# Kernel tuning notes

Measured on AMD Instinct MI355X. Metric: run time of the kernel, lower is better.

The kernel has to match this reference:

```python
import jax, jax.numpy as jnp
import numpy as np

TOKENS = 8192
IN_F = 4096
OUT_F = 4096
QMAX = 127.0  # int8 symmetric quant range
EPS = 1e-8


def setup_inputs() -> dict:
    key = jax.random.key(0)
    k1, k2, k3, k4 = jax.random.split(key, 4)
    x = jax.random.normal(k1, (TOKENS, IN_F), dtype=jnp.float32)
    # Pre-quantized int8 weight [out_features, in_features]
    weight_q = jax.random.randint(k2, (OUT_F, IN_F), -127, 128, dtype=jnp.int8)
    # Per-output-channel weight scales (realistic small magnitudes)
    weight_scale = jax.random.uniform(k3, (OUT_F,), dtype=jnp.float32) * 0.01 + 1e-3
    bias = jax.random.normal(k4, (OUT_F,), dtype=jnp.float32)
    return {"x": x, "weight_q": weight_q, "weight_scale": weight_scale, "bias": bias}


def reference(x, weight_q, weight_scale, bias):
    # Dynamic per-token symmetric int8 activation quantization
    absmax = jnp.max(jnp.abs(x), axis=-1, keepdims=True)           # [T, 1]
    x_scale = jnp.maximum(absmax, EPS) / QMAX                      # [T, 1]
    x_q = jnp.clip(jnp.round(x / x_scale), -QMAX, QMAX).astype(jnp.int8)
    acc = jax.lax.dot_general(
        x_q, weight_q,
        dimension_numbers=(((1,), (1,)), ((), ())),
        preferred_element_type=jnp.int32,
    )
    # Inline dequant: per-token activation scale * per-channel weight scale
    out = acc.astype(jnp.float32) * x_scale * weight_scale[None, :]
    out = out + bias[None, :]
    return out
```

## Files before the change

### kernel.cpp

```cpp
#include <hip/hip_runtime.h>
#include <cstdint>
#include <cstddef>

#define TOKENS 8192
#define IN_F   4096
#define OUT_F  4096
#define QMAXF  127.0f
#define EPSF   1e-8f

typedef int i32x4  __attribute__((ext_vector_type(4)));
typedef int i32x16 __attribute__((ext_vector_type(16)));

#define BKB 64
#define NT  (IN_F / BKB)
#define LDS_BUF   32768
#define NBUF 4
#define LDS_TOTAL (NBUF * LDS_BUF)

__device__ __forceinline__ void gload16(const void* g, void* l) {
    __builtin_amdgcn_global_load_lds(
        (const __attribute__((address_space(1))) void*)g,
        (__attribute__((address_space(3))) void*)l,
        16, 0, 0);
}

__device__ __forceinline__ void bar() {
    asm volatile("" ::: "memory");
    __builtin_amdgcn_s_barrier();
    asm volatile("" ::: "memory");
}

__device__ __forceinline__ int quant1(float v, float inv) {
    int q = (int)rintf(v * inv);
    q = q > 127 ? 127 : q;
    q = q < -127 ? -127 : q;
    return q;
}

__device__ __forceinline__ unsigned int pack4i(int a, int b, int c, int d) {
    return (unsigned int)(a & 255) | ((unsigned int)(b & 255) << 8) |
           ((unsigned int)(c & 255) << 16) | ((unsigned int)(d & 255) << 24);
}

__global__ __launch_bounds__(256) void quant_x_kernel(const float* __restrict__ x,
                                                      signed char* __restrict__ xq,
                                                      float* __restrict__ xscale) {
    const int t   = blockIdx.x;
    const int tid = threadIdx.x;
    const float* xr = x + (size_t)t * IN_F + tid * 16;

    float4 v[4];
    float am = 0.0f;
#pragma unroll
    for (int i = 0; i < 4; ++i) {
        v[i] = ((const float4*)xr)[i];
        am = fmaxf(am, fmaxf(fmaxf(fabsf(v[i].x), fabsf(v[i].y)),
                             fmaxf(fabsf(v[i].z), fabsf(v[i].w))));
    }
#pragma unroll
    for (int off = 32; off >= 1; off >>= 1)
        am = fmaxf(am, __shfl_xor(am, off));

    __shared__ float wmax[4];
    const int wid = tid >> 6, lane = tid & 63;
    if (lane == 0) wmax[wid] = am;
    __syncthreads();
    am = fmaxf(fmaxf(wmax[0], wmax[1]), fmaxf(wmax[2], wmax[3]));

    const float s   = fmaxf(am, EPSF) / QMAXF;
    const float inv = QMAXF / fmaxf(am, EPSF);
    if (tid == 0) xscale[t] = s;

    unsigned int w[4];
#pragma unroll
    for (int i = 0; i < 4; ++i) {
        w[i] = pack4i(quant1(v[i].x, inv), quant1(v[i].y, inv),
                      quant1(v[i].z, inv), quant1(v[i].w, inv));
    }
    *(uint4*)(xq + (size_t)t * IN_F + tid * 16) = make_uint4(w[0], w[1], w[2], w[3]);
}

__global__ __launch_bounds__(256) void pack_w_kernel(const int* __restrict__ w,
                                                     signed char* __restrict__ wq) {
    const size_t idx = (size_t)blockIdx.x * 256 + threadIdx.x;
    const int4* src = (const int4*)w + idx * 4;
    unsigned int o[4];
#pragma unroll
    for (int i = 0; i < 4; ++i) {
        int4 u = src[i];
        o[i] = pack4i(u.x, u.y, u.z, u.w);
    }
    ((uint4*)wq)[idx] = make_uint4(o[0], o[1], o[2], o[3]);
}

__global__ __launch_bounds__(512, 2) void gemm_kernel(const signed char* __restrict__ xq,
                                                      const signed char* __restrict__ wq,
                                                      const float* __restrict__ xscale,
                                                      const float* __restrict__ wscale,
                                                      const float* __restrict__ bias,
                                                      float* __restrict__ out) {
    extern __shared__ __align__(16) char lds[];

    const int tid  = threadIdx.x;
    const int wid  = tid >> 6;
    const int lane = tid & 63;
    const int wr   = wid >> 2;
    const int wc   = wid & 3;
    const int bid  = blockIdx.x;
    const int bm0  = (bid & 31) * 256;
    const int bn0  = (bid >> 5) * 256;

    const int srow = (tid >> 6) * 16 + (tid & 15);
    const int scol = ((tid >> 4) & 3) * 16;
    const signed char* gA0 = xq + (size_t)(bm0 + srow)       * IN_F + scol;
    const signed char* gA1 = xq + (size_t)(bm0 + 128 + srow) * IN_F + scol;
    const signed char* gB0 = wq + (size_t)(bn0 + srow)       * IN_F + scol;
    const signed char* gB1 = wq + (size_t)(bn0 + 128 + srow) * IN_F + scol;
    const int ldst = tid * 16;

    const int l31 = lane & 31, hi = lane >> 5;
    int a_off[4][2], b_off[2][2];
#pragma unroll
    for (int m = 0; m < 4; ++m) {
        const int rw = wr * 8 + m * 2 + (l31 >> 4);
        const int rb = (l31 & 15) * 16;
#pragma unroll
        for (int ks = 0; ks < 2; ++ks)
            a_off[m][ks] = rw * 1024 + (ks * 2 + hi) * 256 + rb;
    }
#pragma unroll
    for (int n = 0; n < 2; ++n) {
        const int rw = wc * 4 + n * 2 + (l31 >> 4);
        const int rb = (l31 & 15) * 16;
#pragma unroll
        for (int ks = 0; ks < 2; ++ks)
            b_off[n][ks] = 16384 + rw * 1024 + (ks * 2 + hi) * 256 + rb;
    }

    i32x16 acc[4][2];
#pragma unroll
    for (int m = 0; m < 4; ++m)
#pragma unroll
        for (int n = 0; n < 2; ++n)
#pragma unroll
            for (int r = 0; r < 16; ++r) acc[m][n][r] = 0;

#pragma unroll
    for (int s = 0; s < 3; ++s) {
        char* S = lds + s * LDS_BUF;
        const int ko = s * BKB;
        gload16(gA0 + ko, S + ldst);
        gload16(gA1 + ko, S + 8192  + ldst);
        gload16(gB0 + ko, S + 16384 + ldst);
        gload16(gB1 + ko, S + 24576 + ldst);
    }
    asm volatile("s_waitcnt vmcnt(4)" ::: "memory");
    bar();

    i32x4 a0[4], b0[2];
#pragma unroll
    for (int m = 0; m < 4; ++m) a0[m] = *(const i32x4*)(lds + a_off[m][0]);
#pragma unroll
    for (int n = 0; n < 2; ++n) b0[n] = *(const i32x4*)(lds + b_off[n][0]);

    for (int t = 0; t < NT; ++t) {
        const char* Ab = lds + (t & 3) * LDS_BUF;
        const char* An = lds + ((t + 1) & 3) * LDS_BUF;
        char* Sd = lds + ((t + 3) & 3) * LDS_BUF;
        const bool st = (t + 3 < NT);
        const int koff = (t + 3) * BKB;

        i32x4 a1[4], b1[2];
#pragma unroll
        for (int m = 0; m < 4; ++m) a1[m] = *(const i32x4*)(Ab + a_off[m][1]);
#pragma unroll
        for (int n = 0; n < 2; ++n) b1[n] = *(const i32x4*)(Ab + b_off[n][1]);
        if (st) {
            gload16(gA0 + koff, Sd + ldst);
            gload16(gB0 + koff, Sd + 16384 + ldst);
        }
        __builtin_amdgcn_s_setprio(1);
#pragma unroll
        for (int m = 0; m < 4; ++m)
#pragma unroll
            for (int n = 0; n < 2; ++n)
                acc[m][n] = __builtin_amdgcn_mfma_i32_32x32x32_i8(a0[m], b0[n], acc[m][n], 0, 0, 0);
        __builtin_amdgcn_s_setprio(0);

        i32x4 a0n[4], b0n[2];
#pragma unroll
        for (int m = 0; m < 4; ++m) a0n[m] = *(const i32x4*)(An + a_off[m][0]);
#pragma unroll
        for (int n = 0; n < 2; ++n) b0n[n] = *(const i32x4*)(An + b_off[n][0]);
        if (st) {
            gload16(gA1 + koff, Sd + 8192  + ldst);
            gload16(gB1 + koff, Sd + 24576 + ldst);
        }
        __builtin_amdgcn_s_setprio(1);
#pragma unroll
        for (int m = 0; m < 4; ++m)
#pragma unroll
            for (int n = 0; n < 2; ++n)
                acc[m][n] = __builtin_amdgcn_mfma_i32_32x32x32_i8(a1[m], b1[n], acc[m][n], 0, 0, 0);
        __builtin_amdgcn_s_setprio(0);

        if (t + 3 < NT) {
            asm volatile("s_waitcnt vmcnt(4)" ::: "memory");
        } else {
            asm volatile("s_waitcnt vmcnt(0)" ::: "memory");
        }
        bar();

#pragma unroll
        for (int m = 0; m < 4; ++m) a0[m] = a0n[m];
#pragma unroll
        for (int n = 0; n < 2; ++n) b0[n] = b0n[n];
    }

#pragma unroll
    for (int m = 0; m < 4; ++m) {
        const int rbase = bm0 + wr * 128 + m * 32 + 4 * hi;
        float xsv[16];
#pragma unroll
        for (int r = 0; r < 16; ++r)
            xsv[r] = xscale[rbase + (r & 3) + 8 * (r >> 2)];
#pragma unroll
        for (int n = 0; n < 2; ++n) {
            const int col = bn0 + wc * 64 + n * 32 + l31;
            const float wsc = wscale[col];
            const float bv  = bias[col];
#pragma unroll
            for (int r = 0; r < 16; ++r) {
                const int row = rbase + (r & 3) + 8 * (r >> 2);
                out[(size_t)row * OUT_F + col] = (float)acc[m][n][r] * xsv[r] * wsc + bv;
            }
        }
    }
}

extern "C" void kernel_launch(void* const* d_in, const int* in_sizes, int n_in,
                              void* d_out, int out_size, void* d_ws, size_t ws_size,
                              hipStream_t stream) {
    const float* x      = (const float*)d_in[0];
    const int*   w      = (const int*)d_in[1];
    const float* wscale = (const float*)d_in[2];
    const float* bias   = (const float*)d_in[3];
    float* out = (float*)d_out;

    char* ws = (char*)d_ws;
    signed char* xq  = (signed char*)ws;
    signed char* wq8 = (signed char*)(ws + (size_t)TOKENS * IN_F);
    float* xscale    = (float*)(ws + (size_t)TOKENS * IN_F + (size_t)OUT_F * IN_F);

    hipFuncSetAttribute((const void*)gemm_kernel,
                        hipFuncAttributeMaxDynamicSharedMemorySize, LDS_TOTAL);

    quant_x_kernel<<<TOKENS, 256, 0, stream>>>(x, xq, xscale);
    pack_w_kernel<<<(OUT_F * (IN_F / 16)) / 256, 256, 0, stream>>>(w, wq8);
    gemm_kernel<<<(TOKENS / 256) * (OUT_F / 256), 512, LDS_TOTAL, stream>>>(
        xq, wq8, xscale, wscale, bias, out);
}
```

Baseline: 208.9 us.

## Shrink GEMM tile to 256x128 with 4 waves, double buffering and block swizzle

```diff
diff --git a/kernel.cpp b/kernel.cpp
--- a/kernel.cpp
+++ b/kernel.cpp
@@ -13,21 +13,14 @@
 
 #define BKB 64
 #define NT  (IN_F / BKB)
-#define LDS_BUF   32768
-#define NBUF 4
-#define LDS_TOTAL (NBUF * LDS_BUF)
+#define ABYTES 16384
+#define BUFB   24576
 
 __device__ __forceinline__ void gload16(const void* g, void* l) {
     __builtin_amdgcn_global_load_lds(
         (const __attribute__((address_space(1))) void*)g,
         (__attribute__((address_space(3))) void*)l,
         16, 0, 0);
-}
-
-__device__ __forceinline__ void bar() {
-    asm volatile("" ::: "memory");
-    __builtin_amdgcn_s_barrier();
-    asm volatile("" ::: "memory");
 }
 
 __device__ __forceinline__ int quant1(float v, float inv) {
@@ -93,48 +86,46 @@
     ((uint4*)wq)[idx] = make_uint4(o[0], o[1], o[2], o[3]);
 }
 
-__global__ __launch_bounds__(512, 2) void gemm_kernel(const signed char* __restrict__ xq,
+__global__ __launch_bounds__(256, 2) void gemm_kernel(const signed char* __restrict__ xq,
                                                       const signed char* __restrict__ wq,
                                                       const float* __restrict__ xscale,
                                                       const float* __restrict__ wscale,
                                                       const float* __restrict__ bias,
                                                       float* __restrict__ out) {
-    extern __shared__ __align__(16) char lds[];
+    __shared__ __align__(16) char lds[2 * BUFB];
 
     const int tid  = threadIdx.x;
     const int wid  = tid >> 6;
     const int lane = tid & 63;
-    const int wr   = wid >> 2;
-    const int wc   = wid & 3;
-    const int bid  = blockIdx.x;
-    const int bm0  = (bid & 31) * 256;
-    const int bn0  = (bid >> 5) * 256;
-
-    const int srow = (tid >> 6) * 16 + (tid & 15);
+    const int wr   = wid >> 1;
+    const int wc   = wid & 1;
+
+    const int bid = blockIdx.x;
+    const int swz = (bid & 7) * 128 + (bid >> 3);
+    const int bm0 = (swz >> 5) * 256;
+    const int bn0 = (swz & 31) * 128;
+
+    const int srow = ((tid >> 6) << 4) + (tid & 15);
     const int scol = ((tid >> 4) & 3) * 16;
-    const signed char* gA0 = xq + (size_t)(bm0 + srow)       * IN_F + scol;
-    const signed char* gA1 = xq + (size_t)(bm0 + 128 + srow) * IN_F + scol;
-    const signed char* gB0 = wq + (size_t)(bn0 + srow)       * IN_F + scol;
-    const signed char* gB1 = wq + (size_t)(bn0 + 128 + srow) * IN_F + scol;
+    const signed char* pA = xq + (size_t)(bm0 + srow) * IN_F + scol;
+    const signed char* pB = wq + (size_t)(bn0 + srow) * IN_F + scol;
     const int ldst = tid * 16;
 
     const int l31 = lane & 31, hi = lane >> 5;
     int a_off[4][2], b_off[2][2];
 #pragma unroll
     for (int m = 0; m < 4; ++m) {
-        const int rw = wr * 8 + m * 2 + (l31 >> 4);
-        const int rb = (l31 & 15) * 16;
+        const int win = wr * 8 + m * 2 + (l31 >> 4);
 #pragma unroll
         for (int ks = 0; ks < 2; ++ks)
-            a_off[m][ks] = rw * 1024 + (ks * 2 + hi) * 256 + rb;
+            a_off[m][ks] = win * 1024 + (ks * 2 + hi) * 256 + (l31 & 15) * 16;
     }
 #pragma unroll
     for (int n = 0; n < 2; ++n) {
-        const int rw = wc * 4 + n * 2 + (l31 >> 4);
-        const int rb = (l31 & 15) * 16;
+        const int win = wc * 4 + n * 2 + (l31 >> 4);
 #pragma unroll
         for (int ks = 0; ks < 2; ++ks)
-            b_off[n][ks] = 16384 + rw * 1024 + (ks * 2 + hi) * 256 + rb;
+            b_off[n][ks] = ABYTES + win * 1024 + (ks * 2 + hi) * 256 + (l31 & 15) * 16;
     }
 
     i32x16 acc[4][2];
@@ -145,76 +136,56 @@
 #pragma unroll
             for (int r = 0; r < 16; ++r) acc[m][n][r] = 0;
 
-#pragma unroll
-    for (int s = 0; s < 3; ++s) {
-        char* S = lds + s * LDS_BUF;
-        const int ko = s * BKB;
-        gload16(gA0 + ko, S + ldst);
-        gload16(gA1 + ko, S + 8192  + ldst);
-        gload16(gB0 + ko, S + 16384 + ldst);
-        gload16(gB1 + ko, S + 24576 + ldst);
-    }
-    asm volatile("s_waitcnt vmcnt(4)" ::: "memory");
-    bar();
-
-    i32x4 a0[4], b0[2];
-#pragma unroll
-    for (int m = 0; m < 4; ++m) a0[m] = *(const i32x4*)(lds + a_off[m][0]);
-#pragma unroll
-    for (int n = 0; n < 2; ++n) b0[n] = *(const i32x4*)(lds + b_off[n][0]);
+    {
+        char* S = lds;
+#pragma unroll
+        for (int c = 0; c < 4; ++c)
+            gload16(pA + (size_t)c * 64 * IN_F, S + c * 4096 + ldst);
+#pragma unroll
+        for (int c = 0; c < 2; ++c)
+            gload16(pB + (size_t)c * 64 * IN_F, S + ABYTES + c * 4096 + ldst);
+    }
+    asm volatile("s_waitcnt vmcnt(0)" ::: "memory");
+    __builtin_amdgcn_s_barrier();
 
     for (int t = 0; t < NT; ++t) {
-        const char* Ab = lds + (t & 3) * LDS_BUF;
-        const char* An = lds + ((t + 1) & 3) * LDS_BUF;
-        char* Sd = lds + ((t + 3) & 3) * LDS_BUF;
-        const bool st = (t + 3 < NT);
-        const int koff = (t + 3) * BKB;
-
-        i32x4 a1[4], b1[2];
-#pragma unroll
-        for (int m = 0; m < 4; ++m) a1[m] = *(const i32x4*)(Ab + a_off[m][1]);
-#pragma unroll
-        for (int n = 0; n < 2; ++n) b1[n] = *(const i32x4*)(Ab + b_off[n][1]);
-        if (st) {
-            gload16(gA0 + koff, Sd + ldst);
-            gload16(gB0 + koff, Sd + 16384 + ldst);
+        const char* Ab = lds + (t & 1) * BUFB;
+
+        if (t + 1 < NT) {
+            char* S = lds + ((t + 1) & 1) * BUFB;
+            const int ko = (t + 1) * BKB;
+#pragma unroll
+            for (int c = 0; c < 4; ++c)
+                gload16(pA + (size_t)c * 64 * IN_F + ko, S + c * 4096 + ldst);
+#pragma unroll
+            for (int c = 0; c < 2; ++c)
+                gload16(pB + (size_t)c * 64 * IN_F + ko, S + ABYTES + c * 4096 + ldst);
         }
+
+        i32x4 b[2][2], a[4][2];
+#pragma unroll
+        for (int n = 0; n < 2; ++n)
+#pragma unroll
+            for (int ks = 0; ks < 2; ++ks)
+                b[n][ks] = *(const i32x4*)(Ab + b_off[n][ks]);
+#pragma unroll
+        for (int m = 0; m < 4; ++m)
+#pragma unroll
+            for (int ks = 0; ks < 2; ++ks)
+                a[m][ks] = *(const i32x4*)(Ab + a_off[m][ks]);
+
         __builtin_amdgcn_s_setprio(1);
 #pragma unroll
         for (int m = 0; m < 4; ++m)
 #pragma unroll
             for (int n = 0; n < 2; ++n)
-                acc[m][n] = __builtin_amdgcn_mfma_i32_32x32x32_i8(a0[m], b0[n], acc[m][n], 0, 0, 0);
+#pragma unroll
+                for (int ks = 0; ks < 2; ++ks)
+                    acc[m][n] = __builtin_amdgcn_mfma_i32_32x32x32_i8(a[m][ks], b[n][ks], acc[m][n], 0, 0, 0);
         __builtin_amdgcn_s_setprio(0);
 
-        i32x4 a0n[4], b0n[2];
-#pragma unroll
-        for (int m = 0; m < 4; ++m) a0n[m] = *(const i32x4*)(An + a_off[m][0]);
-#pragma unroll
-        for (int n = 0; n < 2; ++n) b0n[n] = *(const i32x4*)(An + b_off[n][0]);
-        if (st) {
-            gload16(gA1 + koff, Sd + 8192  + ldst);
-            gload16(gB1 + koff, Sd + 24576 + ldst);
-        }
-        __builtin_amdgcn_s_setprio(1);
-#pragma unroll
-        for (int m = 0; m < 4; ++m)
-#pragma unroll
-            for (int n = 0; n < 2; ++n)
-                acc[m][n] = __builtin_amdgcn_mfma_i32_32x32x32_i8(a1[m], b1[n], acc[m][n], 0, 0, 0);
-        __builtin_amdgcn_s_setprio(0);
-
-        if (t + 3 < NT) {
-            asm volatile("s_waitcnt vmcnt(4)" ::: "memory");
-        } else {
-            asm volatile("s_waitcnt vmcnt(0)" ::: "memory");
-        }
-        bar();
-
-#pragma unroll
-        for (int m = 0; m < 4; ++m) a0[m] = a0n[m];
-#pragma unroll
-        for (int n = 0; n < 2; ++n) b0[n] = b0n[n];
+        asm volatile("s_waitcnt vmcnt(0)" ::: "memory");
+        __builtin_amdgcn_s_barrier();
     }
 
 #pragma unroll
@@ -252,11 +223,8 @@
     signed char* wq8 = (signed char*)(ws + (size_t)TOKENS * IN_F);
     float* xscale    = (float*)(ws + (size_t)TOKENS * IN_F + (size_t)OUT_F * IN_F);
 
-    hipFuncSetAttribute((const void*)gemm_kernel,
-                        hipFuncAttributeMaxDynamicSharedMemorySize, LDS_TOTAL);
-
     quant_x_kernel<<<TOKENS, 256, 0, stream>>>(x, xq, xscale);
     pack_w_kernel<<<(OUT_F * (IN_F / 16)) / 256, 256, 0, stream>>>(w, wq8);
-    gemm_kernel<<<(TOKENS / 256) * (OUT_F / 256), 512, LDS_TOTAL, stream>>>(
+    gemm_kernel<<<(TOKENS / 256) * (OUT_F / 128), 256, 0, stream>>>(
         xq, wq8, xscale, wscale, bias, out);
 }
```

New measurement: 246.1 us. 17.8% more time.
